# Kernel tuning notes

Measured on AMD Instinct MI355X. Metric: run time of the kernel, lower is better.

## Reference

```python
import jax, jax.numpy as jnp
import numpy as np


def _ln(x, g, b):
    m = x.mean(-1, keepdims=True)
    v = ((x - m) ** 2).mean(-1, keepdims=True)
    return (x - m) / jnp.sqrt(v + 1e-5) * g + b


def setup_inputs() -> dict:
    B, N, NC, EC = 4, 512, 128, 32
    KN, KE = 10, 5
    OC = 2 * EC  # NodeEdgeCombiner out_channels = 2*edge_channels
    key = jax.random.key(0)
    ks = jax.random.split(key, 16)
    s = lambda k, *sh: jax.random.normal(k, sh, jnp.float32) * 0.05
    return dict(
        node=jax.random.normal(ks[0], (B, N, NC), jnp.float32),
        edge=jax.random.normal(ks[1], (B, N, N, EC), jnp.float32),
        block_id=jnp.sort(jax.random.randint(ks[2], (B, N), 0, 16), axis=-1),
        virtual_mask=jax.random.bernoulli(ks[3], 0.1, (B, N)),
        W_nt=s(ks[4], 2 * EC + NC, NC), b_nt=jnp.zeros((NC,), jnp.float32),
        W_n1=s(ks[5], NC, 2 * OC), b_n1=jnp.zeros((2 * OC,), jnp.float32),
        W_e1=s(ks[6], EC, OC), b_e1=jnp.zeros((OC,), jnp.float32),
        W_f1=s(ks[7], OC, OC), b_f1=jnp.zeros((OC,), jnp.float32),
        W_f2=s(ks[8], OC, OC), b_f2=jnp.zeros((OC,), jnp.float32),
        W_no1=s(ks[9], NC, NC), b_no1=jnp.zeros((NC,), jnp.float32),
        g_no=jnp.ones((NC,), jnp.float32), be_no=jnp.zeros((NC,), jnp.float32),
        W_no2=s(ks[10], NC, KN), b_no2=jnp.zeros((KN,), jnp.float32),
        W_eo1=s(ks[11], OC, EC), b_eo1=jnp.zeros((EC,), jnp.float32),
        g_eo=jnp.ones((EC,), jnp.float32), be_eo=jnp.zeros((EC,), jnp.float32),
        W_eo2=s(ks[12], EC, KE), b_eo2=jnp.zeros((KE,), jnp.float32),
    )


def reference(node, edge, block_id, virtual_mask,
              W_nt, b_nt, W_n1, b_n1, W_e1, b_e1, W_f1, b_f1, W_f2, b_f2,
              W_no1, b_no1, g_no, be_no, W_no2, b_no2,
              W_eo1, b_eo1, g_eo, be_eo, W_eo2, b_eo2):
    silu = jax.nn.silu
    # masks from block ids
    nm = block_id >= 0                                   # B x N node mask
    bi = block_id[:, :, None]
    bj = block_id[:, None, :]
    pv = nm[:, :, None] & nm[:, None, :]
    # causal block mask: i may see j in strictly earlier blocks, or same block
    # unless i is a virtual (next-block placeholder) node
    causal = pv & ((bi > bj) | ((bi == bj) & ~virtual_mask[:, :, None]))
    em = causal | jnp.swapaxes(causal, 1, 2)             # symmetric edge mask
    nodem = node * nm[..., None]
    edgem = edge * em[..., None]
    # edge_to_node: masked mean of causal incoming & outgoing edges -> 2*EC
    c = causal.astype(edge.dtype)
    x_in = jnp.einsum('bijc,bij->bic', edgem, c) / jnp.maximum(c.sum(2), 1.0)[..., None]
    x_out = jnp.einsum('bjic,bji->bic', edgem, c) / jnp.maximum(c.sum(1), 1.0)[..., None]
    # node_transform: Linear + SiLU, then re-mask
    h = silu(jnp.concatenate([x_in, x_out, nodem], -1) @ W_nt + b_nt) * nm[..., None]
    # NodeEdgeCombiner (simple=False)
    e = edgem @ W_e1 + b_e1                              # B x N x N x OC
    n = h @ W_n1 + b_n1                                  # B x N x 2*OC
    n1, n2 = jnp.split(n, 2, axis=-1)
    npair = n1[:, None, :, :] + n2[:, :, None, :]        # outer-sum: n1[j]+n2[i]
    e = silu(npair + e + silu(npair @ W_f1 + b_f1) * silu(e @ W_f2 + b_f2))
    e = e + jnp.swapaxes(e, 1, 2)                        # symmetrize
    e = e * em[..., None]
    # output MLP heads (Linear -> LN -> SiLU -> Linear), masked
    node_logit = (silu(_ln(h @ W_no1 + b_no1, g_no, be_no)) @ W_no2 + b_no2) * nm[..., None]
    edge_logit = (silu(_ln(e @ W_eo1 + b_eo1, g_eo, be_eo)) @ W_eo2 + b_eo2) * em[..., None]
    return node_logit, edge_logit
```

## Files before the change

kernel.cpp:

```cpp
#include <hip/hip_runtime.h>

#define NQ 512
#define NC 128
#define EC 32
#define OC 64

__device__ __forceinline__ float silu_f(float x) {
    return x / (1.0f + __expf(-x));
}

__global__ void decode_mask_kernel(const unsigned char* __restrict__ raw,
                                   int* __restrict__ out, int n) {
    __shared__ int cntA, cntN;
    int t = threadIdx.x;
    if (t == 0) { cntA = 0; cntN = 0; }
    __syncthreads();
    int la = 0, ln = 0;
    for (int idx = t; idx < n; idx += blockDim.x) {
        unsigned char v = raw[idx];
        if (v) { if ((idx & 3) == 0) la++; else ln++; }
    }
    if (la) atomicAdd(&cntA, la);
    if (ln) atomicAdd(&cntN, ln);
    __syncthreads();
    int a = cntA, nn = cntN;
    for (int i = t; i < n; i += blockDim.x) {
        int v;
        if (a > 0 && nn == 0)      v = ((const int*)raw)[i];
        else if (a == 0)           v = (((const float*)raw)[i] != 0.0f);
        else                       v = (raw[i] != 0);
        out[i] = v;
    }
}

__global__ __launch_bounds__(256) void tile_sum_kernel(
    const float* __restrict__ edge, const int* __restrict__ block_id,
    const int* __restrict__ vmd,
    float* __restrict__ xin_part, float* __restrict__ xout_part) {
    __shared__ float wmask[64][64];
    __shared__ int idI[64], vmI[64], idJ[64], vmJ[64];

    const int t = threadIdx.x;
    const int bid = blockIdx.x;
    const int b = bid >> 6, It = (bid >> 3) & 7, Jt = bid & 7;
    const int I0 = It * 64, J0 = Jt * 64;

    if (t < 64)       { idI[t] = block_id[b * NQ + I0 + t]; vmI[t] = vmd[b * NQ + I0 + t]; }
    else if (t < 128) { int u = t - 64; idJ[u] = block_id[b * NQ + J0 + u]; vmJ[u] = vmd[b * NQ + J0 + u]; }
    __syncthreads();

    for (int idx = t; idx < 4096; idx += 256) {
        int a = idx >> 6, bb = idx & 63;
        int ida = idI[a], idb = idJ[bb];
        bool w = (ida >= 0) && (idb >= 0) &&
                 ((ida > idb) || (ida == idb && !vmI[a]));
        wmask[a][bb] = w ? 1.0f : 0.0f;
    }
    __syncthreads();

    const float* base = edge + (((size_t)(b * NQ) + I0) * NQ + J0) * EC;

    {
        const int bb1 = t >> 3, c0 = (t & 7) * 4;
        float a1x = 0.f, a1y = 0.f, a1z = 0.f, a1w = 0.f;
        float a2x = 0.f, a2y = 0.f, a2z = 0.f, a2w = 0.f;
        for (int a = 0; a < 64; ++a) {
            const float4* row = (const float4*)(base + (size_t)a * NQ * EC);
            float4 v1 = row[t];
            float4 v2 = row[t + 256];
            float w1 = wmask[a][bb1];
            float w2 = wmask[a][bb1 + 32];
            a1x += w1 * v1.x; a1y += w1 * v1.y; a1z += w1 * v1.z; a1w += w1 * v1.w;
            a2x += w2 * v2.x; a2y += w2 * v2.y; a2z += w2 * v2.z; a2w += w2 * v2.w;
        }
        float4 o1 = {a1x, a1y, a1z, a1w};
        float4 o2 = {a2x, a2y, a2z, a2w};
        *(float4*)(xout_part + ((size_t)(b * 8 + It) * NQ + J0 + bb1) * EC + c0) = o1;
        *(float4*)(xout_part + ((size_t)(b * 8 + It) * NQ + J0 + bb1 + 32) * EC + c0) = o2;
    }

    {
        const int c = t & 31, g = t >> 5;
        float acc[8];
        #pragma unroll
        for (int k = 0; k < 8; ++k) acc[k] = 0.0f;
        #pragma unroll 1
        for (int k = 0; k < 8; ++k) {
            const int a = g + 8 * k;
            const float* rowa = base + (size_t)a * NQ * EC + c;
            float s = 0.f;
            #pragma unroll 4
            for (int bb = 0; bb < 64; ++bb) s += wmask[a][bb] * rowa[bb * EC];
            acc[k] = s;
        }
        #pragma unroll
        for (int k = 0; k < 8; ++k) {
            const int a = g + 8 * k;
            xin_part[((size_t)(b * 8 + Jt) * NQ + I0 + a) * EC + c] = acc[k];
        }
    }
}

__global__ __launch_bounds__(128) void node2_kernel(
    const float* __restrict__ node, const int* __restrict__ block_id,
    const int* __restrict__ vmd,
    const float* __restrict__ xin_part, const float* __restrict__ xout_part,
    const float* __restrict__ W_nt, const float* __restrict__ b_nt,
    const float* __restrict__ W_n1, const float* __restrict__ b_n1,
    const float* __restrict__ W_f1, const float* __restrict__ b_f1,
    const float* __restrict__ W_no1, const float* __restrict__ b_no1,
    const float* __restrict__ g_no, const float* __restrict__ be_no,
    const float* __restrict__ W_no2, const float* __restrict__ b_no2,
    float* __restrict__ n_ws, float* __restrict__ q1_ws, float* __restrict__ q2_ws,
    float* __restrict__ out_node) {
    const int bi = blockIdx.x;
    const int b = bi >> 9, i = bi & (NQ - 1);
    const int t = threadIdx.x;

    __shared__ int   sid[NQ];
    __shared__ int   svm[NQ];
    __shared__ int   redi[128], redo[128];
    __shared__ float xcat[192];
    __shared__ float hbuf[128];
    __shared__ float red[128];
    __shared__ float nbuf[128];
    __shared__ float zbuf[128];

    for (int k = t; k < NQ; k += 128) {
        sid[k] = block_id[b * NQ + k];
        svm[k] = vmd[b * NQ + k];
    }
    __syncthreads();

    const int  id_i = sid[i];
    const int  vm_i = svm[i];
    const bool nm_i = (id_i >= 0);

    int ci = 0, co = 0;
    #pragma unroll
    for (int r = 0; r < 4; ++r) {
        int j = t + 128 * r;
        int idj = sid[j];
        bool pv = nm_i && (idj >= 0);
        if (pv && ((id_i > idj) || (id_i == idj && !vm_i)))  ci++;
        if (pv && ((idj > id_i) || (idj == id_i && !svm[j]))) co++;
    }
    redi[t] = ci; redo[t] = co;
    __syncthreads();
    for (int s = 64; s > 0; s >>= 1) {
        if (t < s) { redi[t] += redi[t + s]; redo[t] += redo[t + s]; }
        __syncthreads();
    }
    const float cnt_in  = fmaxf((float)redi[0], 1.0f);
    const float cnt_out = fmaxf((float)redo[0], 1.0f);

    if (t < 32) {
        float s = 0.f;
        #pragma unroll
        for (int q = 0; q < 8; ++q)
            s += xin_part[((size_t)(b * 8 + q) * NQ + i) * EC + t];
        xcat[t] = s / cnt_in;
    } else if (t < 64) {
        int c = t - 32;
        float s = 0.f;
        #pragma unroll
        for (int q = 0; q < 8; ++q)
            s += xout_part[((size_t)(b * 8 + q) * NQ + i) * EC + c];
        xcat[t] = s / cnt_out;
    }
    {
        float nv = node[(size_t)(b * NQ + i) * NC + t];
        xcat[64 + t] = nm_i ? nv : 0.0f;
    }
    __syncthreads();

    float acc = b_nt[t];
    #pragma unroll 4
    for (int k = 0; k < 192; ++k) acc += xcat[k] * W_nt[k * NC + t];
    float h = nm_i ? silu_f(acc) : 0.0f;
    hbuf[t] = h;
    __syncthreads();

    float accn = b_n1[t];
    float u = b_no1[t];
    #pragma unroll 4
    for (int k = 0; k < 128; ++k) {
        float hk = hbuf[k];
        accn += hk * W_n1[k * 128 + t];
        u    += hk * W_no1[k * 128 + t];
    }
    n_ws[(size_t)(b * NQ + i) * 128 + t] = accn;

    nbuf[t] = accn;
    red[t] = u;
    __syncthreads();

    {
        int cc = t & 63;
        const float* src = nbuf + ((t < 64) ? 0 : 64);
        float q = (t < 64) ? 0.0f : b_f1[cc];
        #pragma unroll 4
        for (int k = 0; k < 64; ++k) q += src[k] * W_f1[k * 64 + cc];
        float* dst = (t < 64) ? q1_ws : q2_ws;
        dst[(size_t)(b * NQ + i) * 64 + cc] = q;
    }

    for (int s = 64; s > 0; s >>= 1) { if (t < s) red[t] += red[t + s]; __syncthreads(); }
    float m = red[0] * (1.0f / 128.0f);
    __syncthreads();
    float d = u - m;
    red[t] = d * d;
    __syncthreads();
    for (int s = 64; s > 0; s >>= 1) { if (t < s) red[t] += red[t + s]; __syncthreads(); }
    float var = red[0] * (1.0f / 128.0f);
    float z = silu_f(d * rsqrtf(var + 1e-5f) * g_no[t] + be_no[t]);
    zbuf[t] = z;
    __syncthreads();

    if (t < 10) {
        float o = b_no2[t];
        #pragma unroll 4
        for (int k2 = 0; k2 < 128; ++k2) o += zbuf[k2] * W_no2[k2 * 10 + t];
        out_node[(size_t)(b * NQ + i) * 10 + t] = nm_i ? o : 0.0f;
    }
}

__global__ __launch_bounds__(256, 6) void edge_kernel(
    const float* __restrict__ edge, const int* __restrict__ block_id,
    const int* __restrict__ vmd, const float* __restrict__ n_ws,
    const float* __restrict__ q1_ws, const float* __restrict__ q2_ws,
    const float* __restrict__ W_e1, const float* __restrict__ b_e1,
    const float* __restrict__ W_f2, const float* __restrict__ b_f2,
    const float* __restrict__ W_eo1, const float* __restrict__ b_eo1,
    const float* __restrict__ g_eo, const float* __restrict__ be_eo,
    const float* __restrict__ W_eo2, const float* __restrict__ b_eo2,
    float* __restrict__ out_edge) {
    __shared__ float e0T[64][64];
    __shared__ float smA[32 * 66];
    float* red2 = smA;
    float* oBuf = smA + 512;

    const int tid = threadIdx.x;
    const int p = tid & 63;
    const int w = __builtin_amdgcn_readfirstlane(tid >> 6);
    const int bid = blockIdx.x;

    int b, ib0, jb0;
    bool tail;
    if (bid < 8192) {
        b = bid >> 11;
        int rem = bid & 2047;
        ib0 = rem >> 2;
        jb0 = ib0 + (rem & 3) * 64;
        tail = false;
    } else {
        int t2 = bid - 8192;
        b = t2 >> 2;
        ib0 = (t2 & 3) * 64;
        jb0 = 0;
        tail = true;
    }
    const int i_p = tail ? (ib0 + p) : ib0;
    const int j_p = tail ? (i_p + 256) : ((jb0 + p) & (NQ - 1));

    const float* nb0 = n_ws  + (size_t)b * NQ * 128;
    const float* q1t = q1_ws + (size_t)b * NQ * 64;
    const float* q2t = q2_ws + (size_t)b * NQ * 64;

    float es[16];
    #pragma unroll
    for (int u = 0; u < 16; ++u) es[u] = 0.0f;

    #pragma unroll 1
    for (int d = 0; d < 2; ++d) {
        {
            const int pr = tid >> 2, u = tid & 3;
            const int i_r = tail ? (ib0 + pr) : ib0;
            const int j_r = tail ? (i_r + 256) : ((jb0 + pr) & (NQ - 1));
            const size_t rowbase = d == 0
                ? (((size_t)(b * NQ) + i_r) * NQ + j_r) * EC
                : (((size_t)(b * NQ) + j_r) * NQ + i_r) * EC;
            const float4* src = (const float4*)(edge + rowbase);
            float4 v0 = src[u];
            float4 v1 = src[u + 4];
            smA[(4 * u + 0) * 66 + pr] = v0.x; smA[(4 * u + 1) * 66 + pr] = v0.y;
            smA[(4 * u + 2) * 66 + pr] = v0.z; smA[(4 * u + 3) * 66 + pr] = v0.w;
            smA[(4 * (u + 4) + 0) * 66 + pr] = v1.x; smA[(4 * (u + 4) + 1) * 66 + pr] = v1.y;
            smA[(4 * (u + 4) + 2) * 66 + pr] = v1.z; smA[(4 * (u + 4) + 3) * 66 + pr] = v1.w;
        }
        __syncthreads();

        float e0c[16];
        #pragma unroll
        for (int u = 0; u < 16; ++u) e0c[u] = b_e1[w * 16 + u];
        #pragma unroll 4
        for (int k = 0; k < EC; ++k) {
            float ek = smA[k * 66 + p];
            const float* wr = W_e1 + k * OC + w * 16;
            #pragma unroll
            for (int u = 0; u < 16; ++u) e0c[u] += ek * wr[u];
        }
        #pragma unroll
        for (int u = 0; u < 16; ++u) e0T[w * 16 + u][p] = e0c[u];
        __syncthreads();

        float t2a[16];
        #pragma unroll
        for (int u = 0; u < 16; ++u) t2a[u] = b_f2[w * 16 + u];
        #pragma unroll 4
        for (int k = 0; k < OC; ++k) {
            float e0k = e0T[k][p];
            const float* wr = W_f2 + k * OC + w * 16;
            #pragma unroll
            for (int u = 0; u < 16; ++u) t2a[u] += e0k * wr[u];
        }

        {
            const int ja = d == 0 ? j_p : i_p;
            const int ib = d == 0 ? i_p : j_p;
            const float* pq1 = q1t + (size_t)ja * 64 + w * 16;
            const float* pq2 = q2t + (size_t)ib * 64 + w * 16;
            const float* pn1 = nb0 + (size_t)ja * 128 + w * 16;
            const float* pn2 = nb0 + (size_t)ib * 128 + 64 + w * 16;
            #pragma unroll
            for (int v4 = 0; v4 < 4; ++v4) {
                float4 a1 = ((const float4*)pq1)[v4];
                float4 a2 = ((const float4*)pq2)[v4];
                float4 b1 = ((const float4*)pn1)[v4];
                float4 b2 = ((const float4*)pn2)[v4];
                float q1r[4] = {a1.x, a1.y, a1.z, a1.w};
                float q2r[4] = {a2.x, a2.y, a2.z, a2.w};
                float n1r[4] = {b1.x, b1.y, b1.z, b1.w};
                float n2r[4] = {b2.x, b2.y, b2.z, b2.w};
                #pragma unroll
                for (int r = 0; r < 4; ++r) {
                    int c = v4 * 4 + r;
                    float t1 = silu_f(q1r[r] + q2r[r]);
                    float t2 = silu_f(t2a[c]);
                    es[c] += silu_f(n1r[r] + n2r[r] + e0c[c] + t1 * t2);
                }
            }
        }
        __syncthreads();
    }

    #pragma unroll
    for (int u = 0; u < 16; ++u) e0T[w * 16 + u][p] = es[u];
    __syncthreads();

    const int c0 = w * 8;
    float y[8];
    #pragma unroll
    for (int u = 0; u < 8; ++u) y[u] = b_eo1[c0 + u];
    #pragma unroll 4
    for (int k = 0; k < OC; ++k) {
        float esk = e0T[k][p];
        const float* wr = W_eo1 + k * 32 + c0;
        #pragma unroll
        for (int u = 0; u < 8; ++u) y[u] += esk * wr[u];
    }

    float s1 = 0.f, s2 = 0.f;
    #pragma unroll
    for (int u = 0; u < 8; ++u) { s1 += y[u]; s2 += y[u] * y[u]; }
    red2[0 * 256 + w * 64 + p] = s1;
    red2[1 * 256 + w * 64 + p] = s2;
    __syncthreads();
    float S1 = red2[p] + red2[64 + p] + red2[128 + p] + red2[192 + p];
    float S2 = red2[256 + p] + red2[320 + p] + red2[384 + p] + red2[448 + p];
    float mean = S1 * (1.0f / 32.0f);
    float var  = S2 * (1.0f / 32.0f) - mean * mean;
    float rs = rsqrtf(var + 1e-5f);

    float o[5] = {0.f, 0.f, 0.f, 0.f, 0.f};
    #pragma unroll
    for (int u = 0; u < 8; ++u) {
        float z = silu_f((y[u] - mean) * rs * g_eo[c0 + u] + be_eo[c0 + u]);
        const float* wr = W_eo2 + (c0 + u) * 5;
        #pragma unroll
        for (int q = 0; q < 5; ++q) o[q] += z * wr[q];
    }
    #pragma unroll
    for (int q = 0; q < 5; ++q) oBuf[(w * 64 + p) * 5 + q] = o[q];
    __syncthreads();

    if (w == 0) {
        const int id_i = block_id[b * NQ + i_p], id_j = block_id[b * NQ + j_p];
        const int vm_i = vmd[b * NQ + i_p],      vm_j = vmd[b * NQ + j_p];
        const bool em = (id_i >= 0) && (id_j >= 0) &&
                        ((id_i != id_j) || (!vm_i) || (!vm_j));
        float* oe1 = out_edge + (((size_t)(b * NQ) + i_p) * NQ + j_p) * 5;
        float* oe2 = out_edge + (((size_t)(b * NQ) + j_p) * NQ + i_p) * 5;
        #pragma unroll
        for (int q = 0; q < 5; ++q) {
            float vq = b_eo2[q] + oBuf[(0 * 64 + p) * 5 + q] + oBuf[(1 * 64 + p) * 5 + q]
                                + oBuf[(2 * 64 + p) * 5 + q] + oBuf[(3 * 64 + p) * 5 + q];
            vq = em ? vq : 0.0f;
            oe1[q] = vq;
            oe2[q] = vq;
        }
    }
}

extern "C" void kernel_launch(void* const* d_in, const int* in_sizes, int n_in,
                              void* d_out, int out_size, void* d_ws, size_t ws_size,
                              hipStream_t stream) {
    const float* node     = (const float*)d_in[0];
    const float* edge     = (const float*)d_in[1];
    const int*   block_id = (const int*)d_in[2];
    const void*  vm_raw   = d_in[3];
    const float* W_nt  = (const float*)d_in[4];
    const float* b_nt  = (const float*)d_in[5];
    const float* W_n1  = (const float*)d_in[6];
    const float* b_n1  = (const float*)d_in[7];
    const float* W_e1  = (const float*)d_in[8];
    const float* b_e1  = (const float*)d_in[9];
    const float* W_f1  = (const float*)d_in[10];
    const float* b_f1  = (const float*)d_in[11];
    const float* W_f2  = (const float*)d_in[12];
    const float* b_f2  = (const float*)d_in[13];
    const float* W_no1 = (const float*)d_in[14];
    const float* b_no1 = (const float*)d_in[15];
    const float* g_no  = (const float*)d_in[16];
    const float* be_no = (const float*)d_in[17];
    const float* W_no2 = (const float*)d_in[18];
    const float* b_no2 = (const float*)d_in[19];
    const float* W_eo1 = (const float*)d_in[20];
    const float* b_eo1 = (const float*)d_in[21];
    const float* g_eo  = (const float*)d_in[22];
    const float* be_eo = (const float*)d_in[23];
    const float* W_eo2 = (const float*)d_in[24];
    const float* b_eo2 = (const float*)d_in[25];

    char* ws = (char*)d_ws;
    int*   vmd   = (int*)ws;
    float* n_ws  = (float*)(ws + 8192);
    float* q1_ws = (float*)(ws + 8192 + (1 << 20));
    float* q2_ws = (float*)(ws + 8192 + (1 << 20) + (512 << 10));
    float* xin_part  = (float*)(ws + 8192 + (2 << 20));
    float* xout_part = (float*)(ws + 8192 + (4 << 20));
    float* out_node = (float*)d_out;
    float* out_edge = out_node + 4 * 512 * 10;

    decode_mask_kernel<<<1, 256, 0, stream>>>((const unsigned char*)vm_raw, vmd, 4 * 512);
    tile_sum_kernel<<<256, 256, 0, stream>>>(edge, block_id, vmd, xin_part, xout_part);
    node2_kernel<<<4 * 512, 128, 0, stream>>>(
        node, block_id, vmd, xin_part, xout_part,
        W_nt, b_nt, W_n1, b_n1, W_f1, b_f1, W_no1, b_no1, g_no, be_no, W_no2, b_no2,
        n_ws, q1_ws, q2_ws, out_node);
    edge_kernel<<<8192 + 16, 256, 0, stream>>>(
        edge, block_id, vmd, n_ws, q1_ws, q2_ws,
        W_e1, b_e1, W_f2, b_f2,
        W_eo1, b_eo1, g_eo, be_eo, W_eo2, b_eo2, out_edge);
}
```

Measured before the change: 699.8 us.

## Quadruple tile_sum threads with split row reduction; relax edge_kernel occupancy bound

```diff
diff --git a/kernel.cpp b/kernel.cpp
--- a/kernel.cpp
+++ b/kernel.cpp
@@ -33,12 +33,13 @@
     }
 }
 
-__global__ __launch_bounds__(256) void tile_sum_kernel(
+__global__ __launch_bounds__(1024) void tile_sum_kernel(
     const float* __restrict__ edge, const int* __restrict__ block_id,
     const int* __restrict__ vmd,
     float* __restrict__ xin_part, float* __restrict__ xout_part) {
     __shared__ float wmask[64][64];
     __shared__ int idI[64], vmI[64], idJ[64], vmJ[64];
+    __shared__ float4 partA[512];
 
     const int t = threadIdx.x;
     const int bid = blockIdx.x;
@@ -49,7 +50,7 @@
     else if (t < 128) { int u = t - 64; idJ[u] = block_id[b * NQ + J0 + u]; vmJ[u] = vmd[b * NQ + J0 + u]; }
     __syncthreads();
 
-    for (int idx = t; idx < 4096; idx += 256) {
+    for (int idx = t; idx < 4096; idx += 1024) {
         int a = idx >> 6, bb = idx & 63;
         int ida = idI[a], idb = idJ[bb];
         bool w = (ida >= 0) && (idb >= 0) &&
@@ -61,42 +62,38 @@
     const float* base = edge + (((size_t)(b * NQ) + I0) * NQ + J0) * EC;
 
     {
-        const int bb1 = t >> 3, c0 = (t & 7) * 4;
-        float a1x = 0.f, a1y = 0.f, a1z = 0.f, a1w = 0.f;
-        float a2x = 0.f, a2y = 0.f, a2z = 0.f, a2w = 0.f;
-        for (int a = 0; a < 64; ++a) {
+        const int tc = t & 511;
+        const int h  = t >> 9;
+        const int bb = tc >> 3, c0 = (tc & 7) * 4;
+        float4 acc = {0.f, 0.f, 0.f, 0.f};
+        const int a0 = h * 32;
+        for (int k = 0; k < 32; ++k) {
+            const int a = a0 + k;
             const float4* row = (const float4*)(base + (size_t)a * NQ * EC);
-            float4 v1 = row[t];
-            float4 v2 = row[t + 256];
-            float w1 = wmask[a][bb1];
-            float w2 = wmask[a][bb1 + 32];
-            a1x += w1 * v1.x; a1y += w1 * v1.y; a1z += w1 * v1.z; a1w += w1 * v1.w;
-            a2x += w2 * v2.x; a2y += w2 * v2.y; a2z += w2 * v2.z; a2w += w2 * v2.w;
-        }
-        float4 o1 = {a1x, a1y, a1z, a1w};
-        float4 o2 = {a2x, a2y, a2z, a2w};
-        *(float4*)(xout_part + ((size_t)(b * 8 + It) * NQ + J0 + bb1) * EC + c0) = o1;
-        *(float4*)(xout_part + ((size_t)(b * 8 + It) * NQ + J0 + bb1 + 32) * EC + c0) = o2;
-    }
+            float4 v = row[tc];
+            float w = wmask[a][bb];
+            acc.x += w * v.x; acc.y += w * v.y; acc.z += w * v.z; acc.w += w * v.w;
+        }
+        if (h == 1) partA[tc] = acc;
+        __syncthreads();
+        if (h == 0) {
+            float4 p = partA[tc];
+            acc.x += p.x; acc.y += p.y; acc.z += p.z; acc.w += p.w;
+            *(float4*)(xout_part + ((size_t)(b * 8 + It) * NQ + J0 + bb) * EC + c0) = acc;
+        }
+    }
+    __syncthreads();
 
     {
         const int c = t & 31, g = t >> 5;
-        float acc[8];
-        #pragma unroll
-        for (int k = 0; k < 8; ++k) acc[k] = 0.0f;
-        #pragma unroll 1
-        for (int k = 0; k < 8; ++k) {
-            const int a = g + 8 * k;
+        #pragma unroll
+        for (int half = 0; half < 2; ++half) {
+            const int a = g + 32 * half;
             const float* rowa = base + (size_t)a * NQ * EC + c;
             float s = 0.f;
             #pragma unroll 4
             for (int bb = 0; bb < 64; ++bb) s += wmask[a][bb] * rowa[bb * EC];
-            acc[k] = s;
-        }
-        #pragma unroll
-        for (int k = 0; k < 8; ++k) {
-            const int a = g + 8 * k;
-            xin_part[((size_t)(b * 8 + Jt) * NQ + I0 + a) * EC + c] = acc[k];
+            xin_part[((size_t)(b * 8 + Jt) * NQ + I0 + a) * EC + c] = s;
         }
     }
 }
@@ -225,7 +222,7 @@
     }
 }
 
-__global__ __launch_bounds__(256, 6) void edge_kernel(
+__global__ __launch_bounds__(256, 4) void edge_kernel(
     const float* __restrict__ edge, const int* __restrict__ block_id,
     const int* __restrict__ vmd, const float* __restrict__ n_ws,
     const float* __restrict__ q1_ws, const float* __restrict__ q2_ws,
@@ -443,7 +440,7 @@
     float* out_edge = out_node + 4 * 512 * 10;
 
     decode_mask_kernel<<<1, 256, 0, stream>>>((const unsigned char*)vm_raw, vmd, 4 * 512);
-    tile_sum_kernel<<<256, 256, 0, stream>>>(edge, block_id, vmd, xin_part, xout_part);
+    tile_sum_kernel<<<256, 1024, 0, stream>>>(edge, block_id, vmd, xin_part, xout_part);
     node2_kernel<<<4 * 512, 128, 0, stream>>>(
         node, block_id, vmd, xin_part, xout_part,
         W_nt, b_nt, W_n1, b_n1, W_f1, b_f1, W_no1, b_no1, g_no, be_no, W_no2, b_no2,
```

New measurement: 595.0 us. 15.0% less time.
